# Optimization experiments

Measured on AMD Instinct MI355X. Metric: run time of the kernel, lower is better.

The kernel has to match this reference:

```python
import jax, jax.numpy as jnp
import numpy as np

B, T, E = 4, 2048, 1024
H = 16
D = E // H  # head_dim = 64


def setup_inputs() -> dict:
    key = jax.random.key(0)
    k1, k2, k3 = jax.random.split(key, 3)
    x = jax.random.normal(k1, (B, T, E), dtype=jnp.float32)
    # torch nn.Linear weights: y = x @ W.T ; init scaled like uniform fan_in
    W_qkv = jax.random.normal(k2, (3 * E, E), dtype=jnp.float32) * (E ** -0.5)
    W_out = jax.random.normal(k3, (E, E), dtype=jnp.float32) * (E ** -0.5)
    return {"x": x, "W_qkv": W_qkv, "W_out": W_out}


def reference(x, W_qkv, W_out):
    b, t, c = x.shape
    scale = D ** -0.5
    qkv = jnp.einsum('btc,fc->btf', x, W_qkv)          # [B,T,3E]
    q, k, v = jnp.split(qkv, 3, axis=-1)
    # [B,H,T,D]
    q = q.reshape(b, t, H, D).transpose(0, 2, 1, 3)
    k = k.reshape(b, t, H, D).transpose(0, 2, 1, 3)
    v = v.reshape(b, t, H, D).transpose(0, 2, 1, 3)
    attn = jnp.einsum('bhqd,bhkd->bhqk', q, k) * scale  # [B,H,T,T]
    causal = jnp.triu(jnp.ones((t, t), dtype=bool), k=1)
    attn = jnp.where(causal, -jnp.inf, attn)
    attn = jax.nn.softmax(attn, axis=-1)
    out = jnp.einsum('bhqk,bhkd->bhqd', attn, v)        # [B,H,T,D]
    out = out.transpose(0, 2, 1, 3).reshape(b, t, c)
    return jnp.einsum('btc,oc->bto', out, W_out)
```

## Files before the change

### kernel.cpp

```cpp
#include <hip/hip_runtime.h>

using u16 = unsigned short;
using u32 = unsigned int;
typedef __bf16 bf16;
typedef bf16 bf16x8 __attribute__((ext_vector_type(8)));
typedef u16 u16x8 __attribute__((ext_vector_type(8)));
typedef u16 u16x4 __attribute__((ext_vector_type(4)));
typedef u32 u32x2 __attribute__((ext_vector_type(2)));
typedef float f32x4 __attribute__((ext_vector_type(4)));

#define LDSS 72

__device__ __forceinline__ u16 f2bf(float f) {
  u32 u = __builtin_bit_cast(u32, f);
  u += 0x7FFFu + ((u >> 16) & 1u);
  return (u16)(u >> 16);
}

__device__ __forceinline__ u32 packtrunc(float lo, float hi) {
  return __builtin_amdgcn_perm(__builtin_bit_cast(u32, hi),
                               __builtin_bit_cast(u32, lo), 0x07060302u);
}

__device__ __forceinline__ float fexp2(float x) {
#if __has_builtin(__builtin_amdgcn_exp2f)
  return __builtin_amdgcn_exp2f(x);
#else
  return exp2f(x);
#endif
}

__device__ __forceinline__ bf16x8 ldfrag(const u16* p) {
  return __builtin_bit_cast(bf16x8, *(const u16x8*)p);
}

__device__ __forceinline__ u16x8 cvt8(const float* p) {
  float4 a = ((const float4*)p)[0];
  float4 b = ((const float4*)p)[1];
  u16x8 o;
  o[0] = f2bf(a.x); o[1] = f2bf(a.y); o[2] = f2bf(a.z); o[3] = f2bf(a.w);
  o[4] = f2bf(b.x); o[5] = f2bf(b.y); o[6] = f2bf(b.z); o[7] = f2bf(b.w);
  return o;
}

__device__ __forceinline__ void gll16(const u16* g, u16* l) {
  __builtin_amdgcn_global_load_lds(
      (const __attribute__((address_space(1))) u32*)g,
      (__attribute__((address_space(3))) u32*)l, 16, 0, 0);
}

__global__ __launch_bounds__(256) void cvt_bf16(
    const float* __restrict__ src, u16* __restrict__ dst, int n8) {
  int i = blockIdx.x * 256 + threadIdx.x;
  const int stride = gridDim.x * 256;
  for (; i < n8; i += stride)
    ((u16x8*)dst)[i] = cvt8(&src[(size_t)i * 8]);
}

template<int MODE, int NBX>
__global__ __launch_bounds__(512) void gemm128(
    const u16* __restrict__ Ag, const u16* __restrict__ Bg,
    u16* __restrict__ Qw, u16* __restrict__ Kw, u16* __restrict__ Vtw,
    float* __restrict__ Og) {
  extern __shared__ u16 lds[];
  u16* Ab0 = lds;
  u16* Bb0 = lds + 8192;
  u16* Ab1 = lds + 24576;
  u16* Bb1 = lds + 32768;

  const int tid = threadIdx.x;
  const int lane = tid & 63;
  const int wid = tid >> 6;
  const int wm = wid >> 2, wn = wid & 3;
  const int quad = lane >> 4, l16 = lane & 15;
  const int lr = lane >> 3;
  const int csrc = ((lane & 7) * 8) ^ (lr << 3);
  const int swl = (l16 & 7) << 3;

  const int nwg = NBX * 64;
  const int cpx = nwg >> 3;
  const int bid = blockIdx.x;
  const int swz = (bid & 7) * cpx + (bid >> 3);
  const int by = swz / NBX, bx = swz % NBX;
  const int arow0 = by * 128, brow0 = bx * 256;

  f32x4 acc[4][4] = {};

  auto stg = [&](int t, u16* Abuf, u16* Bbuf) {
#pragma unroll
    for (int s2 = 0; s2 < 2; ++s2) {
      int r = s2 * 64 + wid * 8;
      gll16(&Ag[(size_t)(arow0 + r + lr) * 1024 + t * 64 + csrc], &Abuf[r * 64]);
    }
#pragma unroll
    for (int s2 = 0; s2 < 4; ++s2) {
      int r = s2 * 64 + wid * 8;
      gll16(&Bg[(size_t)(brow0 + r + lr) * 1024 + t * 64 + csrc], &Bbuf[r * 64]);
    }
  };

  stg(0, Ab0, Bb0);

  auto body = [&](const u16* Ac, const u16* Bc, u16* An, u16* Bn, int t) {
    asm volatile("s_waitcnt lgkmcnt(0)" ::: "memory");
    __builtin_amdgcn_s_barrier();
    if (t + 1 < 16) {
      stg(t + 1, An, Bn);
      asm volatile("s_waitcnt vmcnt(6)" ::: "memory");
    } else {
      asm volatile("s_waitcnt vmcnt(0)" ::: "memory");
    }
    __builtin_amdgcn_s_barrier();

    bf16x8 bfx[8], af[4];
#pragma unroll
    for (int j2 = 0; j2 < 4; ++j2)
#pragma unroll
      for (int kk = 0; kk < 2; ++kk)
        bfx[j2 * 2 + kk] = ldfrag(
            &Bc[(wn * 64 + j2 * 16 + l16) * 64 + ((kk * 32 + quad * 8) ^ swl)]);
#pragma unroll
    for (int mh = 0; mh < 2; ++mh) {
#pragma unroll
      for (int i2 = 0; i2 < 2; ++i2)
#pragma unroll
        for (int kk = 0; kk < 2; ++kk)
          af[i2 * 2 + kk] = ldfrag(
              &Ac[(wm * 64 + (mh * 2 + i2) * 16 + l16) * 64 + ((kk * 32 + quad * 8) ^ swl)]);
      __builtin_amdgcn_s_setprio(1);
#pragma unroll
      for (int i2 = 0; i2 < 2; ++i2)
#pragma unroll
        for (int j2 = 0; j2 < 4; ++j2)
#pragma unroll
          for (int kk = 0; kk < 2; ++kk)
            acc[mh * 2 + i2][j2] = __builtin_amdgcn_mfma_f32_16x16x32_bf16(
                af[i2 * 2 + kk], bfx[j2 * 2 + kk], acc[mh * 2 + i2][j2], 0, 0, 0);
      __builtin_amdgcn_s_setprio(0);
    }
  };

  for (int t = 0; t < 16; t += 2) {
    body(Ab0, Bb0, Ab1, Bb1, t);
    body(Ab1, Bb1, Ab0, Bb0, t + 1);
  }

  if constexpr (MODE == 0) {
    const int part = bx >> 2;
    const int h = (bx & 3) * 4 + wn;
    const int bb = by >> 4;
    const int t0 = (by & 15) * 128 + wm * 64;
    if (part < 2) {
      u16* dst = part == 0 ? Qw : Kw;
      const float qs = part == 0 ? 0.18033688011112042f : 1.0f;
      const size_t rowb = (size_t)(bb * 16 + h) * 2048;
#pragma unroll
      for (int i2 = 0; i2 < 4; ++i2)
#pragma unroll
        for (int j2 = 0; j2 < 4; ++j2) {
          int tt = t0 + i2 * 16 + quad * 4;
          int d = j2 * 16 + l16;
#pragma unroll
          for (int r = 0; r < 4; ++r)
            dst[(rowb + tt + r) * 64 + d] = f2bf(acc[i2][j2][r] * qs);
        }
    } else {
      __builtin_amdgcn_s_barrier();
      u16* tb = lds + wid * 4096;
#pragma unroll
      for (int i2 = 0; i2 < 4; ++i2)
#pragma unroll
        for (int j2 = 0; j2 < 4; ++j2) {
          u16x4 v4;
#pragma unroll
          for (int r = 0; r < 4; ++r) v4[r] = f2bf(acc[i2][j2][r]);
          int mb = i2 * 16 + quad * 4;
          *(u16x4*)&tb[(j2 * 16 + l16) * 64 + (mb ^ (l16 << 2))] = v4;
        }
      asm volatile("s_waitcnt lgkmcnt(0)" ::: "memory");
      const int dl = lane;
      const int swr = (dl & 15) << 2;
      u16* vr = Vtw + ((size_t)(bb * 16 + h) * 64 + dl) * 2048 + t0;
#pragma unroll
      for (int c8 = 0; c8 < 8; ++c8) {
        u16x4 q0 = *(u16x4*)&tb[dl * 64 + ((c8 * 8) ^ swr)];
        u16x4 q1 = *(u16x4*)&tb[dl * 64 + ((c8 * 8 + 4) ^ swr)];
        u16x8 o;
        o[0] = q0[0]; o[1] = q0[1]; o[2] = q0[2]; o[3] = q0[3];
        o[4] = q1[0]; o[5] = q1[1]; o[6] = q1[2]; o[7] = q1[3];
        *(u16x8*)&vr[c8 * 8] = o;
      }
    }
  } else {
    const size_t mrow = (size_t)arow0 + wm * 64;
    const int ocol = brow0 + wn * 64;
#pragma unroll
    for (int i2 = 0; i2 < 4; ++i2)
#pragma unroll
      for (int j2 = 0; j2 < 4; ++j2)
#pragma unroll
        for (int r = 0; r < 4; ++r)
          Og[(mrow + i2 * 16 + quad * 4 + r) * 1024 + ocol + j2 * 16 + l16] =
              acc[i2][j2][r];
  }
}

__global__ __launch_bounds__(256) void attn_kernel(
    const u16* __restrict__ Qw, const u16* __restrict__ Kw,
    const u16* __restrict__ Vtw, u16* __restrict__ Ao) {
  __shared__ u16 kbuf0[64 * 64], vbuf0[64 * 64];
  __shared__ u16 kbuf1[64 * 64], vbuf1[64 * 64];
  __shared__ u16 pws[4][32 * LDSS];
  const int tid = threadIdx.x;
  const int lane = tid & 63;
  const int wid = tid >> 6;
  const int quad = lane >> 4;
  const int l16 = lane & 15;
  const int g = 15 - (int)(blockIdx.x >> 6);
  const int bh = blockIdx.x & 63;
  const u16* Qb = Qw + (size_t)bh * 2048 * 64;
  const u16* Kb = Kw + (size_t)bh * 2048 * 64;
  const u16* Vb = Vtw + (size_t)bh * 64 * 2048;
  const int sq = 4 * g + wid;
  const int qrow0 = sq * 32;
  const int nktw = (sq >> 1) + 1;
  const int nkt = 2 * g + 2;
  u16* pw = pws[wid];

  const int lr = lane >> 3;
  const int lsw = ((lane & 7) * 8) ^ (lr << 3);
  const int sx = (l16 & 7) << 3;

  bf16x8 qf[2][2];
#pragma unroll
  for (int i = 0; i < 2; ++i)
#pragma unroll
    for (int kk = 0; kk < 2; ++kk)
      qf[i][kk] = ldfrag(&Qb[(size_t)(qrow0 + i * 16 + l16) * 64 + kk * 32 + quad * 8]);

  f32x4 oacc[4][2] = {};
  float lacc[2] = {0.f, 0.f};
  const f32x4 minit = {-8.f, -8.f, -8.f, -8.f};

  auto stage = [&](int kt, u16* kb, u16* vb) {
    const u16* Kt = Kb + (size_t)kt * 4096;
    const u16* Vt = Vb + kt * 64;
#pragma unroll
    for (int c = 0; c < 2; ++c) {
      int base = wid * 1024 + c * 512;
      int rb = wid * 16 + c * 8;
      gll16(&Kt[(size_t)rb * 64 + lr * 64 + lsw], &kb[base]);
      gll16(&Vt[(size_t)rb * 2048 + lr * 2048 + lsw], &vb[base]);
    }
  };

  stage(0, kbuf0, vbuf0);

  auto body = [&](const u16* kc, const u16* vc, u16* kn, u16* vn, int kt) {
    asm volatile("s_waitcnt lgkmcnt(0)" ::: "memory");
    __builtin_amdgcn_s_barrier();
    const bool more = (kt + 1 < nkt);
    if (more) {
      stage(kt + 1, kn, vn);
      asm volatile("s_waitcnt vmcnt(4)" ::: "memory");
    } else {
      asm volatile("s_waitcnt vmcnt(0)" ::: "memory");
    }
    __builtin_amdgcn_s_barrier();
    if (kt >= nktw) return;

    f32x4 sv[2][4];
#pragma unroll
    for (int i = 0; i < 2; ++i)
#pragma unroll
      for (int j = 0; j < 4; ++j) sv[i][j] = minit;
    __builtin_amdgcn_s_setprio(1);
#pragma unroll
    for (int kk = 0; kk < 2; ++kk) {
      const int cq = (kk * 32 + quad * 8) ^ sx;
      bf16x8 kf[4];
#pragma unroll
      for (int j = 0; j < 4; ++j)
        kf[j] = ldfrag(&kc[(j * 16 + l16) * 64 + cq]);
#pragma unroll
      for (int i = 0; i < 2; ++i)
#pragma unroll
        for (int j = 0; j < 4; ++j)
          sv[i][j] = __builtin_amdgcn_mfma_f32_16x16x32_bf16(kf[j], qf[i][kk], sv[i][j], 0, 0, 0);
    }
    __builtin_amdgcn_s_setprio(0);

    if (kt * 64 + 63 > qrow0) {
#pragma unroll
      for (int i = 0; i < 2; ++i) {
        int q = qrow0 + i * 16 + l16;
#pragma unroll
        for (int j = 0; j < 4; ++j)
#pragma unroll
          for (int r = 0; r < 4; ++r)
            if (kt * 64 + j * 16 + quad * 4 + r > q) sv[i][j][r] = -INFINITY;
      }
    }

#pragma unroll
    for (int i = 0; i < 2; ++i) {
      float rs = 0.f;
#pragma unroll
      for (int j = 0; j < 4; ++j) {
        float p0 = fexp2(sv[i][j][0]);
        float p1 = fexp2(sv[i][j][1]);
        float p2 = fexp2(sv[i][j][2]);
        float p3 = fexp2(sv[i][j][3]);
        rs += (p0 + p1) + (p2 + p3);
        u32x2 pk;
        pk[0] = packtrunc(p0, p1);
        pk[1] = packtrunc(p2, p3);
        *(u32x2*)&pw[(i * 16 + l16) * LDSS + j * 16 + quad * 4] = pk;
      }
      lacc[i] += rs;
    }

#pragma unroll
    for (int kk = 0; kk < 2; ++kk) {
      const int cq = (kk * 32 + quad * 8) ^ sx;
      bf16x8 pf[2];
#pragma unroll
      for (int i = 0; i < 2; ++i)
        pf[i] = ldfrag(&pw[(i * 16 + l16) * LDSS + kk * 32 + quad * 8]);
      __builtin_amdgcn_s_setprio(1);
#pragma unroll
      for (int d = 0; d < 4; ++d) {
        bf16x8 vfd = ldfrag(&vc[(d * 16 + l16) * 64 + cq]);
#pragma unroll
        for (int i = 0; i < 2; ++i)
          oacc[d][i] = __builtin_amdgcn_mfma_f32_16x16x32_bf16(vfd, pf[i], oacc[d][i], 0, 0, 0);
      }
      __builtin_amdgcn_s_setprio(0);
    }
  };

  for (int kt = 0; kt < nkt; kt += 2) {
    body(kbuf0, vbuf0, kbuf1, vbuf1, kt);
    body(kbuf1, vbuf1, kbuf0, vbuf0, kt + 1);
  }

  const int bb = bh >> 4, h = bh & 15;
#pragma unroll
  for (int i = 0; i < 2; ++i) {
    float l = lacc[i];
    l += __shfl_xor(l, 16);
    l += __shfl_xor(l, 32);
    float inv = 1.f / l;
#pragma unroll
    for (int d = 0; d < 4; ++d) {
      u16x4 ok;
#pragma unroll
      for (int r = 0; r < 4; ++r) ok[r] = f2bf(oacc[d][i][r] * inv);
      *(u16x4*)&pw[(i * 16 + l16) * LDSS + d * 16 + quad * 4] = ok;
    }
  }
  __builtin_amdgcn_s_waitcnt(0);
  const int row = lane >> 1, half = lane & 1;
  const int t = qrow0 + row;
#pragma unroll
  for (int c = 0; c < 4; ++c) {
    u16x8 v = *(u16x8*)&pw[row * LDSS + half * 32 + c * 8];
    *(u16x8*)&Ao[((size_t)(bb * 2048 + t)) * 1024 + h * 64 + half * 32 + c * 8] = v;
  }
}

extern "C" void kernel_launch(void* const* d_in, const int* in_sizes, int n_in,
                              void* d_out, int out_size, void* d_ws, size_t ws_size,
                              hipStream_t stream) {
  (void)in_sizes; (void)n_in; (void)out_size; (void)ws_size;
  const float* x    = (const float*)d_in[0];
  const float* Wqkv = (const float*)d_in[1];
  const float* Wout = (const float*)d_in[2];
  float* out = (float*)d_out;
  u16* ws = (u16*)d_ws;

  const size_t NX   = (size_t)4 * 2048 * 1024;
  const size_t NQKV = (size_t)3072 * 1024;
  const size_t NOUT = (size_t)1024 * 1024;
  const size_t SZ   = NX;

  u16* Xc    = ws;
  u16* Wqkvc = Xc + NX;
  u16* Woutc = Wqkvc + NQKV;
  u16* Qw    = Woutc + NOUT;
  u16* Kw    = Qw + SZ;
  u16* Vtw   = Kw + SZ;
  u16* Ao    = Vtw + SZ;

  static bool attr_done = false;
  if (!attr_done) {
    (void)hipFuncSetAttribute(reinterpret_cast<const void*>(&gemm128<0, 12>),
                              hipFuncAttributeMaxDynamicSharedMemorySize, 98304);
    (void)hipFuncSetAttribute(reinterpret_cast<const void*>(&gemm128<1, 4>),
                              hipFuncAttributeMaxDynamicSharedMemorySize, 98304);
    attr_done = true;
  }

  cvt_bf16<<<dim3(1024), 256, 0, stream>>>(x, Xc, (int)(NX / 8));
  cvt_bf16<<<dim3(384), 256, 0, stream>>>(Wqkv, Wqkvc, (int)(NQKV / 8));
  cvt_bf16<<<dim3(128), 256, 0, stream>>>(Wout, Woutc, (int)(NOUT / 8));

  gemm128<0, 12><<<dim3(768), 512, 98304, stream>>>(
      Xc, Wqkvc, Qw, Kw, Vtw, nullptr);
  attn_kernel<<<dim3(1024), 256, 0, stream>>>(Qw, Kw, Vtw, Ao);
  gemm128<1, 4><<<dim3(256), 512, 98304, stream>>>(
      Ao, Woutc, nullptr, nullptr, nullptr, out);
}
```

Baseline: 234.1 us.

## Shrink GEMM tiles to 128x128 with 4 waves and fuse conversion kernels

The GEMM tile changes from 128x256 with 8 waves to 128x128 with 4 waves. This doubles the grid size and cuts LDS use to 64KB, which should allow more blocks per CU and better tail balance. The staging loops, vmcnt threshold and epilogue head mapping are updated to match. The three fp32-to-bf16 conversion launches are merged into one kernel that dispatches on index range, saving launch overhead. The trade-off is less operand reuse per tile and more global traffic for the B operand.

```diff
diff --git a/kernel.cpp b/kernel.cpp
--- a/kernel.cpp
+++ b/kernel.cpp
@@ -49,29 +49,37 @@
       (__attribute__((address_space(3))) u32*)l, 16, 0, 0);
 }
 
-__global__ __launch_bounds__(256) void cvt_bf16(
-    const float* __restrict__ src, u16* __restrict__ dst, int n8) {
+__global__ __launch_bounds__(256) void cvt_all(
+    const float* __restrict__ x, const float* __restrict__ wqkv,
+    const float* __restrict__ wout, u16* __restrict__ dst,
+    int nx8, int nq8, int no8) {
   int i = blockIdx.x * 256 + threadIdx.x;
   const int stride = gridDim.x * 256;
-  for (; i < n8; i += stride)
-    ((u16x8*)dst)[i] = cvt8(&src[(size_t)i * 8]);
+  const int total = nx8 + nq8 + no8;
+  for (; i < total; i += stride) {
+    const float* src; int j;
+    if (i < nx8)            { src = x;    j = i; }
+    else if (i < nx8 + nq8) { src = wqkv; j = i - nx8; }
+    else                    { src = wout; j = i - nx8 - nq8; }
+    ((u16x8*)dst)[i] = cvt8(&src[(size_t)j * 8]);
+  }
 }
 
 template<int MODE, int NBX>
-__global__ __launch_bounds__(512) void gemm128(
+__global__ __launch_bounds__(256) void gemm128b(
     const u16* __restrict__ Ag, const u16* __restrict__ Bg,
     u16* __restrict__ Qw, u16* __restrict__ Kw, u16* __restrict__ Vtw,
     float* __restrict__ Og) {
   extern __shared__ u16 lds[];
   u16* Ab0 = lds;
   u16* Bb0 = lds + 8192;
-  u16* Ab1 = lds + 24576;
-  u16* Bb1 = lds + 32768;
+  u16* Ab1 = lds + 16384;
+  u16* Bb1 = lds + 24576;
 
   const int tid = threadIdx.x;
   const int lane = tid & 63;
   const int wid = tid >> 6;
-  const int wm = wid >> 2, wn = wid & 3;
+  const int wm = wid >> 1, wn = wid & 1;
   const int quad = lane >> 4, l16 = lane & 15;
   const int lr = lane >> 3;
   const int csrc = ((lane & 7) * 8) ^ (lr << 3);
@@ -82,19 +90,19 @@
   const int bid = blockIdx.x;
   const int swz = (bid & 7) * cpx + (bid >> 3);
   const int by = swz / NBX, bx = swz % NBX;
-  const int arow0 = by * 128, brow0 = bx * 256;
+  const int arow0 = by * 128, brow0 = bx * 128;
 
   f32x4 acc[4][4] = {};
 
   auto stg = [&](int t, u16* Abuf, u16* Bbuf) {
 #pragma unroll
-    for (int s2 = 0; s2 < 2; ++s2) {
-      int r = s2 * 64 + wid * 8;
+    for (int s2 = 0; s2 < 4; ++s2) {
+      int r = s2 * 32 + wid * 8;
       gll16(&Ag[(size_t)(arow0 + r + lr) * 1024 + t * 64 + csrc], &Abuf[r * 64]);
     }
 #pragma unroll
     for (int s2 = 0; s2 < 4; ++s2) {
-      int r = s2 * 64 + wid * 8;
+      int r = s2 * 32 + wid * 8;
       gll16(&Bg[(size_t)(brow0 + r + lr) * 1024 + t * 64 + csrc], &Bbuf[r * 64]);
     }
   };
@@ -106,7 +114,7 @@
     __builtin_amdgcn_s_barrier();
     if (t + 1 < 16) {
       stg(t + 1, An, Bn);
-      asm volatile("s_waitcnt vmcnt(6)" ::: "memory");
+      asm volatile("s_waitcnt vmcnt(8)" ::: "memory");
     } else {
       asm volatile("s_waitcnt vmcnt(0)" ::: "memory");
     }
@@ -146,8 +154,8 @@
   }
 
   if constexpr (MODE == 0) {
-    const int part = bx >> 2;
-    const int h = (bx & 3) * 4 + wn;
+    const int part = bx >> 3;
+    const int h = (bx & 7) * 2 + wn;
     const int bb = by >> 4;
     const int t0 = (by & 15) * 128 + wm * 64;
     if (part < 2) {
@@ -394,20 +402,19 @@
 
   static bool attr_done = false;
   if (!attr_done) {
-    (void)hipFuncSetAttribute(reinterpret_cast<const void*>(&gemm128<0, 12>),
-                              hipFuncAttributeMaxDynamicSharedMemorySize, 98304);
-    (void)hipFuncSetAttribute(reinterpret_cast<const void*>(&gemm128<1, 4>),
-                              hipFuncAttributeMaxDynamicSharedMemorySize, 98304);
+    (void)hipFuncSetAttribute(reinterpret_cast<const void*>(&gemm128b<0, 24>),
+                              hipFuncAttributeMaxDynamicSharedMemorySize, 65536);
+    (void)hipFuncSetAttribute(reinterpret_cast<const void*>(&gemm128b<1, 8>),
+                              hipFuncAttributeMaxDynamicSharedMemorySize, 65536);
     attr_done = true;
   }
 
-  cvt_bf16<<<dim3(1024), 256, 0, stream>>>(x, Xc, (int)(NX / 8));
-  cvt_bf16<<<dim3(384), 256, 0, stream>>>(Wqkv, Wqkvc, (int)(NQKV / 8));
-  cvt_bf16<<<dim3(128), 256, 0, stream>>>(Wout, Woutc, (int)(NOUT / 8));
-
-  gemm128<0, 12><<<dim3(768), 512, 98304, stream>>>(
+  cvt_all<<<dim3(2048), 256, 0, stream>>>(
+      x, Wqkv, Wout, ws, (int)(NX / 8), (int)(NQKV / 8), (int)(NOUT / 8));
+
+  gemm128b<0, 24><<<dim3(1536), 256, 65536, stream>>>(
       Xc, Wqkvc, Qw, Kw, Vtw, nullptr);
   attn_kernel<<<dim3(1024), 256, 0, stream>>>(Qw, Kw, Vtw, Ao);
-  gemm128<1, 4><<<dim3(256), 512, 98304, stream>>>(
+  gemm128b<1, 8><<<dim3(512), 256, 65536, stream>>>(
       Ao, Woutc, nullptr, nullptr, nullptr, out);
 }
```

New measurement: 235.7 us. About the same (+0.7%).
